# Kernel optimization log

Hardware: AMD Instinct MI355X
Metric: run time of the kernel (lower is better)

## Reference

```python
import jax, jax.numpy as jnp
import numpy as np

B, T, I = 32, 128, 512
H, L, O = 512, 2, 512


def _uniform(key, shape, std):
    return jax.random.uniform(key, shape, jnp.float32, -std, std)


def setup_inputs() -> dict:
    key = jax.random.key(0)
    ks = jax.random.split(key, 12)
    std = 1.0 / np.sqrt(H)
    inp = {
        "x": jax.random.normal(ks[0], (B, T, I), jnp.float32),
        # stacked params: [L, 2, ...]; dir 0 = forward cells, dir 1 = reverse cells
        "Wxh": _uniform(ks[1], (L, 2, I, 2 * H), std),
        "bxh": _uniform(ks[2], (L, 2, 2 * H), std),
        "Whh": _uniform(ks[3], (L, 2, H, 2 * H), std),
        "bhh": _uniform(ks[4], (L, 2, 2 * H), std),
        "Wxr": _uniform(ks[5], (L, 2, I, H), std),
        "bxr": _uniform(ks[6], (L, 2, H), std),
        "Whr": _uniform(ks[7], (L, 2, H, H), std),
        "bhr": _uniform(ks[8], (L, 2, H, ), std),
        "Wfc": _uniform(ks[9], (2 * H, O), 1.0 / np.sqrt(2 * H)),
        "bfc": _uniform(ks[10], (O,), 1.0 / np.sqrt(2 * H)),
    }
    return inp


def gru_layer(seq, Wxh_l, bxh_l, Whh_l, bhh_l, Wxr_l, bxr_l, Whr_l, bhr_l):
    # seq: [T, B, I]. Precompute input projections for all timesteps (one big GEMM),
    # then scan the sequential h-dependent part.
    xh = jnp.einsum('tbi,ih->tbh', seq, Wxh_l) + bxh_l  # [T,B,2H]
    xr = jnp.einsum('tbi,ih->tbh', seq, Wxr_l) + bxr_l  # [T,B,H]

    def step(h, inp):
        xh_t, xr_t = inp
        zr = xh_t + h @ Whh_l + bhh_l
        z, r = jnp.split(zr, 2, axis=-1)
        z = jax.nn.sigmoid(z)
        r = jax.nn.sigmoid(r)
        g = jnp.tanh((h @ Whr_l + bhr_l) * r + xr_t)
        h = z * h + (1.0 - z) * g
        return h, h

    h0 = jnp.zeros((seq.shape[1], Whh_l.shape[0]), seq.dtype)
    _, out = jax.lax.scan(step, h0, (xh, xr))
    return out  # [T,B,H]


def reference(x, Wxh, bxh, Whh, bhh, Wxr, bxr, Whr, bhr, Wfc, bfc):
    # Faithful translation of BidirRecurrentModel.forward (GRU mode):
    # forward stream scans time-ordered input; reverse stream independently scans
    # the time-reversed input (the two streams are NOT concatenated between layers).
    seq_f = jnp.transpose(x, (1, 0, 2))   # [T,B,I]
    seq_r = seq_f[::-1]                   # reversed time order
    n_layers = Wxh.shape[0]
    for l in range(n_layers):
        seq_f = gru_layer(seq_f, Wxh[l, 0], bxh[l, 0], Whh[l, 0], bhh[l, 0],
                          Wxr[l, 0], bxr[l, 0], Whr[l, 0], bhr[l, 0])
        seq_r = gru_layer(seq_r, Wxh[l, 1], bxh[l, 1], Whh[l, 1], bhh[l, 1],
                          Wxr[l, 1], bxr[l, 1], Whr[l, 1], bhr[l, 1])
    # out = last fwd timestep; out_rev = FIRST element of reverse-ordered stream
    # (i.e. the reverse cell's state after one step), exactly as in the source.
    out = jnp.concatenate([seq_f[-1], seq_r[0]], axis=1)  # [B, 2H]
    return out @ Wfc + bfc  # [B, O]
```

## Files before the change

### kernel.cpp

```cpp
#include <hip/hip_runtime.h>
#include <hip/hip_bf16.h>

#define PROJ_ELEMS 12582912
#define SEQ_ELEMS  4194304
#define SLAB_PER_BLK 6144

__global__ __launch_bounds__(256)
void proj_kernel(const float* __restrict__ src,
                 const float* __restrict__ Wxh, const float* __restrict__ bxh,
                 const float* __restrict__ Wxr, const float* __restrict__ bxr,
                 __hip_bfloat16* __restrict__ proj, int layer)
{
    __shared__ float As[32][137];
    __shared__ float Ws[32][132];
    const int tid  = threadIdx.x;
    const int col0 = blockIdx.x * 128;
    const int row0 = blockIdx.y * 128;
    const int d    = row0 >> 12;
    const int ld   = layer * 2 + d;
    const int tx = tid & 15, ty = tid >> 4;

    const bool is_xr = (col0 >= 1024);
    const float* Wbase = is_xr ? (Wxr + (size_t)ld * 512 * 512 + (col0 - 1024))
                               : (Wxh + (size_t)ld * 512 * 1024 + col0);
    const int wstride = is_xr ? 512 : 1024;
    const float* bias = is_xr ? (bxr + ld * 512 + (col0 - 1024))
                              : (bxh + ld * 1024 + col0);

    float acc[8][8];
    #pragma unroll
    for (int i = 0; i < 8; i++)
        #pragma unroll
        for (int j = 0; j < 8; j++) acc[i][j] = 0.f;

    for (int k0 = 0; k0 < 512; k0 += 32) {
        #pragma unroll
        for (int v = 0; v < 4; v++) {
            int idx = tid + v * 256;
            int r   = idx >> 3;
            int c4  = (idx & 7) << 2;
            int gm  = row0 + r;
            int rr  = gm & 4095;
            int tt  = rr >> 5, bb = rr & 31;
            const float* p;
            if (layer == 0) {
                int ts = (gm >= 4096) ? (127 - tt) : tt;
                p = src + ((size_t)bb * 128 + ts) * 512 + (k0 + c4);
            } else {
                p = src + (((size_t)(gm >> 12) * 128 + tt) * 32 + bb) * 512 + (k0 + c4);
            }
            float4 vv = *(const float4*)p;
            As[c4 + 0][r] = vv.x; As[c4 + 1][r] = vv.y;
            As[c4 + 2][r] = vv.z; As[c4 + 3][r] = vv.w;
        }
        #pragma unroll
        for (int v = 0; v < 4; v++) {
            int idx = tid + v * 256;
            int kr  = idx >> 5;
            int c4  = (idx & 31) << 2;
            *(float4*)&Ws[kr][c4] = *(const float4*)(Wbase + (size_t)(k0 + kr) * wstride + c4);
        }
        __syncthreads();
        #pragma unroll
        for (int kk = 0; kk < 32; kk++) {
            float a[8], w[8];
            *(float4*)&a[0] = *(const float4*)&As[kk][ty * 8];
            *(float4*)&a[4] = *(const float4*)&As[kk][ty * 8 + 4];
            *(float4*)&w[0] = *(const float4*)&Ws[kk][tx * 8];
            *(float4*)&w[4] = *(const float4*)&Ws[kk][tx * 8 + 4];
            #pragma unroll
            for (int i = 0; i < 8; i++)
                #pragma unroll
                for (int j = 0; j < 8; j++)
                    acc[i][j] += a[i] * w[j];
        }
        __syncthreads();
    }
    #pragma unroll
    for (int i = 0; i < 8; i++) {
        int gm = row0 + ty * 8 + i;
        __hip_bfloat16* dst = proj + (size_t)gm * 1536 + col0 + tx * 8;
        #pragma unroll
        for (int j = 0; j < 8; j++)
            dst[j] = __float2bfloat16(acc[i][j] + bias[tx * 8 + j]);
    }
}

__global__ __launch_bounds__(256)
void repack_kernel(const float* __restrict__ Whh, const float* __restrict__ Whr,
                   float* __restrict__ slabs)
{
    const int blk = blockIdx.x;
    const int ld = blk >> 7, jb = blk & 127;
    const float* WhhL = Whh + (size_t)ld * 512 * 1024;
    const float* WhrL = Whr + (size_t)ld * 512 * 512;
    float* out = slabs + (size_t)blk * SLAB_PER_BLK;
    for (int u = 0; u < 24; u++) {
        int idx = threadIdx.x + u * 256;
        int rec = idx / 12, r3 = idx % 12;
        int g = rec >> 2, cg = rec & 3;
        int e = r3 >> 2, ki = r3 & 3;
        int k = g * 4 + ki, j = jb * 4 + cg;
        float v;
        if (e == 0)      v = WhhL[(size_t)k * 1024 + j];
        else if (e == 1) v = WhhL[(size_t)k * 1024 + 512 + j];
        else             v = WhrL[(size_t)k * 512 + j];
        out[idx] = v;
    }
}

__global__ __launch_bounds__(256)
void step_kernel(const __hip_bfloat16* __restrict__ proj, float* __restrict__ seq,
                 const float* __restrict__ slabs,
                 const float* __restrict__ bhh, const float* __restrict__ bhr,
                 int layer, int t)
{
    __shared__ __align__(16) float hs[32 * 512];
    const int tid = threadIdx.x;
    const int d   = blockIdx.x >> 7;
    const int jb  = blockIdx.x & 127;
    const int ld  = layer * 2 + d;
    const int cg  = tid & 3;
    const int kh  = (tid >> 2) & 1;
    const int b   = tid >> 3;
    const int j   = jb * 4 + cg;
    const int sb  = b & 7;

    float az = 0.f, ar = 0.f, ag = 0.f;
    float hv_self = 0.f;

    if (t > 0) {
        const float* hsrc = seq + ((size_t)(d * 128 + (t - 1)) * 32) * 512;
        #pragma unroll
        for (int v = 0; v < 16; v++) {
            int id = tid + v * 256;
            int bb = id >> 7, g = id & 127;
            float4 hv = *(const float4*)(hsrc + (size_t)id * 4);
            *(float4*)&hs[bb * 512 + ((g ^ (bb & 7)) << 2)] = hv;
        }
        __syncthreads();

        const float4* wrec = (const float4*)slabs + (size_t)(ld * 128 + jb) * 1536;
        #pragma unroll 4
        for (int gg = 0; gg < 64; gg++) {
            int g = kh * 64 + gg;
            float4 h4 = *(const float4*)&hs[b * 512 + ((g ^ sb) << 2)];
            const float4* wp = wrec + (size_t)(g * 4 + cg) * 3;
            float4 wz = wp[0], wr = wp[1], wg = wp[2];
            az += h4.x * wz.x + h4.y * wz.y + h4.z * wz.z + h4.w * wz.w;
            ar += h4.x * wr.x + h4.y * wr.y + h4.z * wr.z + h4.w * wr.w;
            ag += h4.x * wg.x + h4.y * wg.y + h4.z * wg.z + h4.w * wg.w;
        }
        az += __shfl_xor(az, 4, 64);
        ar += __shfl_xor(ar, 4, 64);
        ag += __shfl_xor(ag, 4, 64);
        hv_self = hs[b * 512 + ((jb ^ sb) << 2) + cg];
    }

    const size_t pb = ((size_t)(d * 128 + t) * 32 + b) * 1536;
    float pz = __bfloat162float(proj[pb + j]);
    float pr = __bfloat162float(proj[pb + 512 + j]);
    float pg = __bfloat162float(proj[pb + 1024 + j]);
    float bz = bhh[ld * 1024 + j];
    float br = bhh[ld * 1024 + 512 + j];
    float bg = bhr[ld * 512 + j];
    float z  = 1.f / (1.f + __expf(-(az + pz + bz)));
    float r  = 1.f / (1.f + __expf(-(ar + pr + br)));
    float gt = tanhf((ag + bg) * r + pg);
    float hn = z * hv_self + (1.f - z) * gt;
    if (kh == 0)
        seq[((size_t)(d * 128 + t) * 32 + b) * 512 + j] = hn;
}

__global__ __launch_bounds__(256)
void fc_kernel(const float* __restrict__ seq, const float* __restrict__ Wfc,
               const float* __restrict__ bfc, float* __restrict__ out)
{
    int idx = blockIdx.x * 256 + threadIdx.x;
    int b = idx >> 9, o = idx & 511;
    const float* catf = seq + ((size_t)(0 * 128 + 127) * 32 + b) * 512;
    const float* catr = seq + ((size_t)(1 * 128 + 0) * 32 + b) * 512;
    float acc = bfc[o];
    #pragma unroll 8
    for (int k = 0; k < 512; k++) acc += catf[k] * Wfc[(size_t)k * 512 + o];
    #pragma unroll 8
    for (int k = 0; k < 512; k++) acc += catr[k] * Wfc[(size_t)(512 + k) * 512 + o];
    out[(size_t)b * 512 + o] = acc;
}

extern "C" void kernel_launch(void* const* d_in, const int* in_sizes, int n_in,
                              void* d_out, int out_size, void* d_ws, size_t ws_size,
                              hipStream_t stream) {
    (void)in_sizes; (void)n_in; (void)out_size; (void)ws_size;
    const float* x   = (const float*)d_in[0];
    const float* Wxh = (const float*)d_in[1];
    const float* bxh = (const float*)d_in[2];
    const float* Whh = (const float*)d_in[3];
    const float* bhh = (const float*)d_in[4];
    const float* Wxr = (const float*)d_in[5];
    const float* bxr = (const float*)d_in[6];
    const float* Whr = (const float*)d_in[7];
    const float* bhr = (const float*)d_in[8];
    const float* Wfc = (const float*)d_in[9];
    const float* bfc = (const float*)d_in[10];
    float* out = (float*)d_out;

    char* base = (char*)d_ws;
    __hip_bfloat16* proj = (__hip_bfloat16*)base;
    float* seq   = (float*)(base + (size_t)PROJ_ELEMS * 2);
    float* slabs = seq + SEQ_ELEMS;

    repack_kernel<<<512, 256, 0, stream>>>(Whh, Whr, slabs);

    dim3 pgrid(12, 64);
    proj_kernel<<<pgrid, 256, 0, stream>>>(x, Wxh, bxh, Wxr, bxr, proj, 0);
    for (int t = 0; t < 128; t++)
        step_kernel<<<256, 256, 0, stream>>>(proj, seq, slabs, bhh, bhr, 0, t);
    proj_kernel<<<pgrid, 256, 0, stream>>>(seq, Wxh, bxh, Wxr, bxr, proj, 1);
    for (int t = 0; t < 128; t++)
        step_kernel<<<256, 256, 0, stream>>>(proj, seq, slabs, bhh, bhr, 1, t);
    fc_kernel<<<64, 256, 0, stream>>>(seq, Wfc, bfc, out);
}
```

Baseline: 2.709 ms.

## Fuse per-timestep GRU launches into one persistent cooperative kernel with grid sync

Replaces the 128 per-timestep step kernel launches per layer with a single cooperative kernel that loops over time and uses a grid-wide barrier between steps. Bias loads and base pointers are hoisted out of the time loop. This removes kernel launch overhead on the sequential recurrence. In exchange it relies on all 256 blocks being co-resident, and grid sync latency is paid per step.

```diff
diff --git a/kernel.cpp b/kernel.cpp
--- a/kernel.cpp
+++ b/kernel.cpp
@@ -1,5 +1,8 @@
 #include <hip/hip_runtime.h>
 #include <hip/hip_bf16.h>
+#include <hip/hip_cooperative_groups.h>
+
+namespace coopg = cooperative_groups;
 
 #define PROJ_ELEMS 12582912
 #define SEQ_ELEMS  4194304
@@ -110,66 +113,77 @@
 }
 
 __global__ __launch_bounds__(256)
-void step_kernel(const __hip_bfloat16* __restrict__ proj, float* __restrict__ seq,
-                 const float* __restrict__ slabs,
-                 const float* __restrict__ bhh, const float* __restrict__ bhr,
-                 int layer, int t)
-{
+void gru_seq_kernel(const __hip_bfloat16* __restrict__ proj, float* __restrict__ seq,
+                    const float* __restrict__ slabs,
+                    const float* __restrict__ bhh, const float* __restrict__ bhr,
+                    int layer)
+{
+    coopg::grid_group grid = coopg::this_grid();
     __shared__ __align__(16) float hs[32 * 512];
     const int tid = threadIdx.x;
     const int d   = blockIdx.x >> 7;
     const int jb  = blockIdx.x & 127;
     const int ld  = layer * 2 + d;
-    const int cg  = tid & 3;
+    const int cgi = tid & 3;
     const int kh  = (tid >> 2) & 1;
     const int b   = tid >> 3;
-    const int j   = jb * 4 + cg;
+    const int j   = jb * 4 + cgi;
     const int sb  = b & 7;
 
-    float az = 0.f, ar = 0.f, ag = 0.f;
-    float hv_self = 0.f;
-
-    if (t > 0) {
-        const float* hsrc = seq + ((size_t)(d * 128 + (t - 1)) * 32) * 512;
-        #pragma unroll
-        for (int v = 0; v < 16; v++) {
-            int id = tid + v * 256;
-            int bb = id >> 7, g = id & 127;
-            float4 hv = *(const float4*)(hsrc + (size_t)id * 4);
-            *(float4*)&hs[bb * 512 + ((g ^ (bb & 7)) << 2)] = hv;
+    const float4* wrec = (const float4*)slabs + (size_t)(ld * 128 + jb) * 1536;
+    const float bz = bhh[ld * 1024 + j];
+    const float br = bhh[ld * 1024 + 512 + j];
+    const float bg = bhr[ld * 512 + j];
+    const float* hbase = seq + (size_t)(d * 128) * 32 * 512;
+    const __hip_bfloat16* pbase = proj + ((size_t)(d * 128) * 32 + b) * 1536 + j;
+    float* wout = seq + ((size_t)(d * 128) * 32 + b) * 512 + j;
+
+    for (int t = 0; t < 128; ++t) {
+        if (t > 0) {
+            const float* hsrc = hbase + (size_t)(t - 1) * 32 * 512;
+            #pragma unroll
+            for (int v = 0; v < 16; v++) {
+                int id = tid + v * 256;
+                int bb = id >> 7, g = id & 127;
+                float4 hv = *(const float4*)(hsrc + (size_t)id * 4);
+                *(float4*)&hs[bb * 512 + ((g ^ (bb & 7)) << 2)] = hv;
+            }
         }
         __syncthreads();
 
-        const float4* wrec = (const float4*)slabs + (size_t)(ld * 128 + jb) * 1536;
-        #pragma unroll 4
-        for (int gg = 0; gg < 64; gg++) {
-            int g = kh * 64 + gg;
-            float4 h4 = *(const float4*)&hs[b * 512 + ((g ^ sb) << 2)];
-            const float4* wp = wrec + (size_t)(g * 4 + cg) * 3;
-            float4 wz = wp[0], wr = wp[1], wg = wp[2];
-            az += h4.x * wz.x + h4.y * wz.y + h4.z * wz.z + h4.w * wz.w;
-            ar += h4.x * wr.x + h4.y * wr.y + h4.z * wr.z + h4.w * wr.w;
-            ag += h4.x * wg.x + h4.y * wg.y + h4.z * wg.z + h4.w * wg.w;
-        }
-        az += __shfl_xor(az, 4, 64);
-        ar += __shfl_xor(ar, 4, 64);
-        ag += __shfl_xor(ag, 4, 64);
-        hv_self = hs[b * 512 + ((jb ^ sb) << 2) + cg];
-    }
-
-    const size_t pb = ((size_t)(d * 128 + t) * 32 + b) * 1536;
-    float pz = __bfloat162float(proj[pb + j]);
-    float pr = __bfloat162float(proj[pb + 512 + j]);
-    float pg = __bfloat162float(proj[pb + 1024 + j]);
-    float bz = bhh[ld * 1024 + j];
-    float br = bhh[ld * 1024 + 512 + j];
-    float bg = bhr[ld * 512 + j];
-    float z  = 1.f / (1.f + __expf(-(az + pz + bz)));
-    float r  = 1.f / (1.f + __expf(-(ar + pr + br)));
-    float gt = tanhf((ag + bg) * r + pg);
-    float hn = z * hv_self + (1.f - z) * gt;
-    if (kh == 0)
-        seq[((size_t)(d * 128 + t) * 32 + b) * 512 + j] = hn;
+        const __hip_bfloat16* pp = pbase + (size_t)t * 32 * 1536;
+        float pz = __bfloat162float(pp[0]);
+        float pr = __bfloat162float(pp[512]);
+        float pg = __bfloat162float(pp[1024]);
+
+        float az = 0.f, ar = 0.f, ag = 0.f;
+        float hv_self = 0.f;
+        if (t > 0) {
+            #pragma unroll 4
+            for (int gg = 0; gg < 64; gg++) {
+                int g = kh * 64 + gg;
+                float4 h4 = *(const float4*)&hs[b * 512 + ((g ^ sb) << 2)];
+                const float4* wp = wrec + (size_t)(g * 4 + cgi) * 3;
+                float4 wz = wp[0], wr = wp[1], wg = wp[2];
+                az += h4.x * wz.x + h4.y * wz.y + h4.z * wz.z + h4.w * wz.w;
+                ar += h4.x * wr.x + h4.y * wr.y + h4.z * wr.z + h4.w * wr.w;
+                ag += h4.x * wg.x + h4.y * wg.y + h4.z * wg.z + h4.w * wg.w;
+            }
+            az += __shfl_xor(az, 4, 64);
+            ar += __shfl_xor(ar, 4, 64);
+            ag += __shfl_xor(ag, 4, 64);
+            hv_self = hs[b * 512 + ((jb ^ sb) << 2) + cgi];
+        }
+
+        float z  = 1.f / (1.f + __expf(-(az + pz + bz)));
+        float r  = 1.f / (1.f + __expf(-(ar + pr + br)));
+        float gt = tanhf((ag + bg) * r + pg);
+        float hn = z * hv_self + (1.f - z) * gt;
+        if (kh == 0)
+            wout[(size_t)t * 32 * 512] = hn;
+
+        grid.sync();
+    }
 }
 
 __global__ __launch_bounds__(256)
@@ -214,10 +228,20 @@
 
     dim3 pgrid(12, 64);
     proj_kernel<<<pgrid, 256, 0, stream>>>(x, Wxh, bxh, Wxr, bxr, proj, 0);
-    for (int t = 0; t < 128; t++)
-        step_kernel<<<256, 256, 0, stream>>>(proj, seq, slabs, bhh, bhr, 0, t);
+    {
+        int layer = 0;
+        void* args[] = {(void*)&proj, (void*)&seq, (void*)&slabs,
+                        (void*)&bhh, (void*)&bhr, (void*)&layer};
+        hipLaunchCooperativeKernel((void*)gru_seq_kernel, dim3(256), dim3(256),
+                                   args, 0, stream);
+    }
     proj_kernel<<<pgrid, 256, 0, stream>>>(seq, Wxh, bxh, Wxr, bxr, proj, 1);
-    for (int t = 0; t < 128; t++)
-        step_kernel<<<256, 256, 0, stream>>>(proj, seq, slabs, bhh, bhr, 1, t);
+    {
+        int layer = 1;
+        void* args[] = {(void*)&proj, (void*)&seq, (void*)&slabs,
+                        (void*)&bhh, (void*)&bhr, (void*)&layer};
+        hipLaunchCooperativeKernel((void*)gru_seq_kernel, dim3(256), dim3(256),
+                                   args, 0, stream);
+    }
     fc_kernel<<<64, 256, 0, stream>>>(seq, Wfc, bfc, out);
 }
```

Result: slower. 9.674 ms (+257.2%).
